# Kernel tuning notes

Hardware: AMD Instinct MI355X
Metric: run time of the kernel (lower is better)

## Reference

```python
import jax, jax.numpy as jnp
import numpy as np

NUM_GROUPS = 32
EPS = 1e-5


def group_norm(x, gamma, beta):
    b, c, h, w = x.shape
    xg = x.reshape(b, NUM_GROUPS, c // NUM_GROUPS, h, w)
    mu = xg.mean(axis=(2, 3, 4), keepdims=True)
    var = xg.var(axis=(2, 3, 4), keepdims=True)
    xg = (xg - mu) * jax.lax.rsqrt(var + EPS)
    x = xg.reshape(b, c, h, w)
    return x * gamma[None, :, None, None] + beta[None, :, None, None]


def conv1x1(x, w, b):
    # 1x1 conv == per-pixel matmul over channels
    return jnp.einsum('oc,bchw->bohw', w, x) + b[None, :, None, None]


def setup_inputs() -> dict:
    key = jax.random.key(0)
    ks = jax.random.split(key, 6)
    c = 512
    scale = 0.02  # keep logits in a sane range
    return {
        'x': jax.random.normal(ks[0], (2, c, 64, 64), dtype=jnp.float32),
        'gn_w': jnp.ones((c,), jnp.float32),
        'gn_b': jnp.zeros((c,), jnp.float32),
        'wq': jax.random.normal(ks[1], (c, c), jnp.float32) * scale,
        'bq': jnp.zeros((c,), jnp.float32),
        'wk': jax.random.normal(ks[2], (c, c), jnp.float32) * scale,
        'bk': jnp.zeros((c,), jnp.float32),
        'wv': jax.random.normal(ks[3], (c, c), jnp.float32) * scale,
        'bv': jnp.zeros((c,), jnp.float32),
        'wo': jax.random.normal(ks[4], (c, c), jnp.float32) * scale,
        'bo': jnp.zeros((c,), jnp.float32),
    }


def reference(x, gn_w, gn_b, wq, bq, wk, bk, wv, bv, wo, bo):
    b, c, h, w = x.shape
    n = h * w
    h_ = group_norm(x, gn_w, gn_b)
    q = conv1x1(h_, wq, bq).reshape(b, c, n)  # (b,c,n)
    k = conv1x1(h_, wk, bk).reshape(b, c, n)
    v = conv1x1(h_, wv, bv).reshape(b, c, n)
    # scores: (b, n_q, n_k) = q^T k, scaled by c^-0.5
    scores = jnp.einsum('bcq,bck->bqk', q, k) * (c ** -0.5)
    attn = jax.nn.softmax(scores, axis=-1)
    # h_ = v @ attn^T  -> (b, c, n_q)
    out = jnp.einsum('bck,bqk->bcq', v, attn).reshape(b, c, h, w)
    return x + conv1x1(out, wo, bo)
```

## Files before the change

### kernel.cpp

```cpp
#include <hip/hip_runtime.h>

typedef __bf16 bf16_t;
typedef __bf16 bf16x8 __attribute__((ext_vector_type(8)));
typedef __bf16 bf16x4 __attribute__((ext_vector_type(4)));
typedef float  floatx4 __attribute__((ext_vector_type(4)));

#define B_  2
#define C_  512
#define N_  4096
#define EPS 1e-5f
#define SCALE 0.044194173824159216f

__device__ __forceinline__ void gl2lds16(const void* g, void* l) {
  __builtin_amdgcn_global_load_lds(
      (const __attribute__((address_space(1))) void*)g,
      (__attribute__((address_space(3))) void*)l, 16, 0, 0);
}

__device__ __forceinline__ unsigned char f8(float x) {
  return (unsigned char)(__builtin_amdgcn_cvt_pk_fp8_f32(x, x, 0, false) & 0xff);
}

template <int BM, int BN>
__device__ __forceinline__ void gemm_main(
    const bf16_t* __restrict__ A, const bf16_t* __restrict__ B, int K,
    int m0, int n0, floatx4 (&acc)[BM / 32][BN / 32],
    bf16_t* __restrict__ As, bf16_t* __restrict__ Bs) {
  const int tid = threadIdx.x;
  const int w = tid >> 6, l = tid & 63;
  const int wm = (w >> 1) * (BM / 2), wn = (w & 1) * (BN / 2);
  const int lrow = l & 15, lq = l >> 4;
  const int key = lrow & 7;
  const int slot0 = lq ^ key;
  const int slot1 = (4 + lq) ^ key;

  floatx4 zero = {0.f, 0.f, 0.f, 0.f};
#pragma unroll
  for (int mm = 0; mm < BM / 32; mm++)
#pragma unroll
    for (int nn = 0; nn < BN / 32; nn++) acc[mm][nn] = zero;

  for (int k0 = 0; k0 < K; k0 += 64) {
#pragma unroll
    for (int p = 0; p < BM / 32; p++) {
      int gch = p * 256 + tid;
      int r = gch >> 3;
      int cg = (gch & 7) ^ (r & 7);
      gl2lds16(A + (size_t)(m0 + r) * K + k0 + cg * 8, As + gch * 8);
    }
#pragma unroll
    for (int p = 0; p < BN / 32; p++) {
      int gch = p * 256 + tid;
      int r = gch >> 3;
      int cg = (gch & 7) ^ (r & 7);
      gl2lds16(B + (size_t)(n0 + r) * K + k0 + cg * 8, Bs + gch * 8);
    }
    __syncthreads();

    bf16x8 af[BM / 32][2], bfr[BN / 32][2];
#pragma unroll
    for (int mm = 0; mm < BM / 32; mm++) {
      int row = wm + mm * 16 + lrow;
      af[mm][0] = *(const bf16x8*)(As + row * 64 + slot0 * 8);
      af[mm][1] = *(const bf16x8*)(As + row * 64 + slot1 * 8);
    }
#pragma unroll
    for (int nn = 0; nn < BN / 32; nn++) {
      int row = wn + nn * 16 + lrow;
      bfr[nn][0] = *(const bf16x8*)(Bs + row * 64 + slot0 * 8);
      bfr[nn][1] = *(const bf16x8*)(Bs + row * 64 + slot1 * 8);
    }
#pragma unroll
    for (int h = 0; h < 2; h++)
#pragma unroll
      for (int mm = 0; mm < BM / 32; mm++)
#pragma unroll
        for (int nn = 0; nn < BN / 32; nn++)
          acc[mm][nn] = __builtin_amdgcn_mfma_f32_16x16x32_bf16(
              af[mm][h], bfr[nn][h], acc[mm][nn], 0, 0, 0);
    __syncthreads();
  }
}

__global__ __launch_bounds__(256) void gemm_qkv(
    const bf16_t* __restrict__ Wqkv, const bf16_t* __restrict__ h_t,
    bf16_t* __restrict__ q_t, bf16_t* __restrict__ k_t,
    unsigned char* __restrict__ v8,
    const float* __restrict__ bq, const float* __restrict__ bk,
    const float* __restrict__ bv) {
  __shared__ __align__(16) char smem[32768];
  floatx4 acc[4][4];
  const int m0 = blockIdx.y * 128, n0 = blockIdx.x * 128;
  gemm_main<128, 128>(Wqkv, h_t, 512, m0, n0, acc,
                      (bf16_t*)smem, (bf16_t*)(smem + 16384));

  const int tid = threadIdx.x, w = tid >> 6, l = tid & 63;
  const int wm = (w >> 1) * 64, wn = (w & 1) * 64;
  const int lrow = l & 15, q4 = (l >> 4) * 4;
  const int mat = m0 >> 9;
  const float* bias = (mat == 0) ? bq : (mat == 1) ? bk : bv;

  if (mat < 2) {
    bf16_t* ot = (mat == 0) ? q_t : k_t;
#pragma unroll
    for (int mm = 0; mm < 4; mm++) {
#pragma unroll
      for (int nn = 0; nn < 4; nn++) {
        int n = n0 + wn + nn * 16 + lrow;
        int mloc = m0 - mat * 512 + wm + mm * 16 + q4;
        floatx4 a = acc[mm][nn];
        bf16x4 t;
#pragma unroll
        for (int r = 0; r < 4; r++) t[r] = (bf16_t)(a[r] + bias[mloc + r]);
        *(bf16x4*)(ot + (size_t)n * 512 + mloc) = t;
      }
    }
  } else {
    unsigned char* tile8 = (unsigned char*)smem;
#pragma unroll
    for (int mm = 0; mm < 4; mm++) {
#pragma unroll
      for (int nn = 0; nn < 4; nn++) {
        int colp = wn + nn * 16 + lrow;
        floatx4 a = acc[mm][nn];
#pragma unroll
        for (int r = 0; r < 4; r++) {
          int row = wm + mm * 16 + q4 + r;
          int ch = (colp >> 4) ^ ((row >> 2) & 7);
          tile8[row * 128 + ch * 16 + (colp & 15)] =
              f8(a[r] + bias[m0 - 1024 + row]);
        }
      }
    }
    __syncthreads();
    const int bb = n0 >> 12, nl0 = n0 & 4095;
    const int mloc0 = m0 - 1024;
#pragma unroll
    for (int i = 0; i < 4; i++) {
      int c = i * 256 + tid;
      int row = c >> 3, k = c & 7;
      int ch = k ^ ((row >> 2) & 7);
      uint4 d = *(const uint4*)(tile8 + row * 128 + ch * 16);
      *(uint4*)(v8 + (size_t)bb * (C_ * N_) + (size_t)(mloc0 + row) * N_ +
                nl0 + k * 16) = d;
    }
  }
}

__global__ __launch_bounds__(256) void gemm_scores(
    const bf16_t* __restrict__ q_t, const bf16_t* __restrict__ k_t,
    unsigned char* __restrict__ S8, size_t sstride, float* __restrict__ L,
    int zbase, int nz) {
  __shared__ __align__(16) char smem[32768];
  const int id = blockIdx.x;
  const int x = id & 7, s = id >> 3;
  const int mi = s & 3, n = (s >> 2) & 31;
  const int zloc = (nz == 2) ? (s >> 7) : 0;
  const int z = (nz == 2) ? zloc : zbase;
  const int m = x * 4 + mi;

  const bf16_t* A = k_t + (size_t)z * (N_ * C_);
  const bf16_t* B = q_t + (size_t)z * (N_ * C_);
  unsigned char* Sb = S8 + (size_t)zloc * sstride;
  float* Lb = L + (size_t)zloc * N_;
  floatx4 acc[4][4];
  const int m0 = m * 128, n0 = n * 128;
  gemm_main<128, 128>(A, B, 512, m0, n0, acc,
                      (bf16_t*)smem, (bf16_t*)(smem + 16384));

  const int tid = threadIdx.x, w = tid >> 6, l = tid & 63;
  const int wm = (w >> 1) * 64, wn = (w & 1) * 64;
  const int lrow = l & 15, lq = l >> 4;

  float lsum[4] = {0.f, 0.f, 0.f, 0.f};
#pragma unroll
  for (int mm = 0; mm < 4; mm++) {
#pragma unroll
    for (int nn = 0; nn < 4; nn++) {
      int i  = n0 + wn + nn * 16 + lrow;
      int jb = m0 + wm + mm * 16 + lq * 4;
      floatx4 a = acc[mm][nn];
      float e0 = __expf(a[0] * SCALE);
      float e1 = __expf(a[1] * SCALE);
      float e2 = __expf(a[2] * SCALE);
      float e3 = __expf(a[3] * SCALE);
      lsum[nn] += (e0 + e1) + (e2 + e3);
      unsigned int p = __builtin_amdgcn_cvt_pk_fp8_f32(e0, e1, 0, false);
      p = __builtin_amdgcn_cvt_pk_fp8_f32(e2, e3, p, true);
      *(unsigned int*)(Sb + (size_t)i * N_ + jb) = p;
    }
  }
#pragma unroll
  for (int nn = 0; nn < 4; nn++) {
    float vsum = lsum[nn];
    vsum += __shfl_xor(vsum, 16);
    vsum += __shfl_xor(vsum, 32);
    if (lq == 0)
      atomicAdd(Lb + n0 + wn + nn * 16 + lrow, vsum);
  }
}

__global__ __launch_bounds__(512) void gemm_pv(
    const unsigned char* __restrict__ S8, size_t sstride,
    const unsigned char* __restrict__ v8, const float* __restrict__ L,
    bf16_t* __restrict__ O_t, int zbase, int nz) {
  __shared__ __align__(16) char smem[49152];
  const int id = blockIdx.x;
  int nb, mb, zloc;
  if (nz == 2) { nb = id >> 6; int g = id & 63; mb = g >> 1; zloc = g & 1; }
  else         { nb = id >> 5; mb = id & 31; zloc = 0; }
  const int z = (nz == 2) ? zloc : zbase;

  const unsigned char* A = S8 + (size_t)zloc * sstride;
  const unsigned char* B = v8 + (size_t)z * (C_ * N_);
  const float* Lb = L + (size_t)zloc * N_;
  const int m0 = mb * 128, n0 = nb * 64;

  const int tid = threadIdx.x;
  const int w = tid >> 6, l = tid & 63;
  const int wk = w >> 2;
  const int wl = w & 3;
  const int t2 = tid & 255;
  unsigned char* Ah = (unsigned char*)smem + wk * (128 * 128);
  unsigned char* Bh = (unsigned char*)(smem + 32768) + wk * (64 * 128);

  const int wm = (wl >> 1) * 64, wn = (wl & 1) * 32;
  const int lrow = l & 15, lq = l >> 4;
  const int key = lrow & 7;
  const int fsub = (lq & 1) * 8;
  const int fc0 = ((0 + (lq >> 1)) ^ key) * 16 + fsub;
  const int fc1 = ((2 + (lq >> 1)) ^ key) * 16 + fsub;
  const int fc2 = ((4 + (lq >> 1)) ^ key) * 16 + fsub;
  const int fc3 = ((6 + (lq >> 1)) ^ key) * 16 + fsub;
  const int fo[4] = {fc0, fc1, fc2, fc3};

  floatx4 acc[4][2];
  floatx4 zero = {0.f, 0.f, 0.f, 0.f};
#pragma unroll
  for (int mm = 0; mm < 4; mm++)
#pragma unroll
    for (int nn = 0; nn < 2; nn++) acc[mm][nn] = zero;

  const int kbase = wk * 2048;
  for (int kk = 0; kk < 2048; kk += 128) {
    const int k0 = kbase + kk;
#pragma unroll
    for (int p = 0; p < 4; p++) {
      int gch = p * 256 + t2;
      int r = gch >> 3;
      int cg = (gch & 7) ^ (r & 7);
      gl2lds16(A + (size_t)(m0 + r) * 4096 + k0 + cg * 16, Ah + gch * 16);
    }
#pragma unroll
    for (int p = 0; p < 2; p++) {
      int gch = p * 256 + t2;
      int r = gch >> 3;
      int cg = (gch & 7) ^ (r & 7);
      gl2lds16(B + (size_t)(n0 + r) * 4096 + k0 + cg * 16, Bh + gch * 16);
    }
    __syncthreads();

    long af[4][4], bfr[2][4];
#pragma unroll
    for (int mm = 0; mm < 4; mm++) {
      int row = wm + mm * 16 + lrow;
#pragma unroll
      for (int h = 0; h < 4; h++)
        af[mm][h] = *(const long*)(Ah + row * 128 + fo[h]);
    }
#pragma unroll
    for (int nn = 0; nn < 2; nn++) {
      int row = wn + nn * 16 + lrow;
#pragma unroll
      for (int h = 0; h < 4; h++)
        bfr[nn][h] = *(const long*)(Bh + row * 128 + fo[h]);
    }
#pragma unroll
    for (int h = 0; h < 4; h++)
#pragma unroll
      for (int mm = 0; mm < 4; mm++)
#pragma unroll
        for (int nn = 0; nn < 2; nn++)
          acc[mm][nn] = __builtin_amdgcn_mfma_f32_16x16x32_fp8_fp8(
              af[mm][h], bfr[nn][h], acc[mm][nn], 0, 0, 0);
    __syncthreads();
  }

  floatx4* buf = (floatx4*)smem;
  const int lanebase = wl * 64 + l;
  if (wk == 1) {
#pragma unroll
    for (int mm = 0; mm < 4; mm++)
#pragma unroll
      for (int nn = 0; nn < 2; nn++)
        buf[(mm * 2 + nn) * 256 + lanebase] = acc[mm][nn];
  }
  __syncthreads();

  bf16_t* tile = (bf16_t*)(smem + 32768);
  if (wk == 0) {
    const int q4 = lq * 4;
#pragma unroll
    for (int mm = 0; mm < 4; mm++) {
      const int rowb = wm + mm * 16 + q4;
      float rv0 = 1.0f / Lb[m0 + rowb + 0];
      float rv1 = 1.0f / Lb[m0 + rowb + 1];
      float rv2 = 1.0f / Lb[m0 + rowb + 2];
      float rv3 = 1.0f / Lb[m0 + rowb + 3];
#pragma unroll
      for (int nn = 0; nn < 2; nn++) {
        floatx4 a = acc[mm][nn] + buf[(mm * 2 + nn) * 256 + lanebase];
        a[0] *= rv0; a[1] *= rv1; a[2] *= rv2; a[3] *= rv3;
        int colp = wn + nn * 16 + lrow;
#pragma unroll
        for (int r = 0; r < 4; r++) {
          int row = rowb + r;
          int ch = (colp >> 3) ^ ((row >> 2) & 7);
          tile[row * 64 + ch * 8 + (colp & 7)] = (bf16_t)a[r];
        }
      }
    }
  }
  __syncthreads();
#pragma unroll
  for (int i = 0; i < 2; i++) {
    int c = i * 512 + tid;
    int row = c >> 3, k = c & 7;
    int ch = k ^ ((row >> 2) & 7);
    bf16x8 d = *(const bf16x8*)(tile + row * 64 + ch * 8);
    *(bf16x8*)(O_t + ((size_t)z * N_ + m0 + row) * C_ + n0 + k * 8) = d;
  }
}

__global__ __launch_bounds__(256) void gemm_final(
    const bf16_t* __restrict__ wo, const bf16_t* __restrict__ O_t,
    const float* __restrict__ bo, const float* __restrict__ x,
    float* __restrict__ out) {
  __shared__ __align__(16) char smem[32768];
  floatx4 acc[2][4];
  const int m0 = blockIdx.y * 64, n0 = blockIdx.x * 128;
  gemm_main<64, 128>(wo, O_t, 512, m0, n0, acc,
                     (bf16_t*)smem, (bf16_t*)(smem + 8192));

  const int tid = threadIdx.x, w = tid >> 6, l = tid & 63;
  const int wm = (w >> 1) * 32, wn = (w & 1) * 64;
  const int lrow = l & 15, q4 = (l >> 4) * 4;

  float* tile = (float*)smem;
#pragma unroll
  for (int mm = 0; mm < 2; mm++) {
#pragma unroll
    for (int nn = 0; nn < 4; nn++) {
      int colp = wn + nn * 16 + lrow;
      floatx4 a = acc[mm][nn];
#pragma unroll
      for (int r = 0; r < 4; r++) {
        int row = wm + mm * 16 + q4 + r;
        int ch = (colp >> 2) ^ ((row >> 2) & 31);
        tile[row * 128 + ch * 4 + (colp & 3)] = a[r] + bo[m0 + row];
      }
    }
  }
  __syncthreads();
  const int bb = n0 >> 12, nl0 = n0 & 4095;
#pragma unroll
  for (int i = 0; i < 8; i++) {
    int c = i * 256 + tid;
    int row = c >> 5, k = c & 31;
    int ch = k ^ ((row >> 2) & 31);
    float4 dv = *(const float4*)(tile + row * 128 + ch * 4);
    size_t off = ((size_t)(bb * C_ + m0 + row)) * N_ + nl0 + k * 4;
    float4 xv = *(const float4*)(x + off);
    dv.x += xv.x; dv.y += xv.y; dv.z += xv.z; dv.w += xv.w;
    *(float4*)(out + off) = dv;
  }
}

__global__ __launch_bounds__(256) void prep_kernel(
    const float* __restrict__ s0, const float* __restrict__ s1,
    const float* __restrict__ s2, const float* __restrict__ s3,
    bf16_t* __restrict__ d_qkv, bf16_t* __restrict__ d_o,
    const float* __restrict__ x, float2* __restrict__ part,
    float* __restrict__ L) {
  const int id = blockIdx.x;
  const int tid = threadIdx.x;
  __shared__ float rs[4], rss[4];
  if (id < 4096) {
    int i = id * 256 + tid;
    int mat = i >> 18, idx = i & 262143;
    const float* s = (mat == 0) ? s0 : (mat == 1) ? s1 : (mat == 2) ? s2 : s3;
    if (mat < 3)
      d_qkv[mat * 262144 + idx] = (bf16_t)s[idx];
    else
      d_o[idx] = (bf16_t)s[idx];
  } else if (id < 4608) {
    const int sid = id - 4096;
    const float4* xp = (const float4*)(x + (size_t)sid * 8192);
    float s = 0.f, ss = 0.f;
#pragma unroll
    for (int i = 0; i < 8; i++) {
      float4 v = xp[tid + i * 256];
      s += v.x + v.y + v.z + v.w;
      ss += v.x * v.x + v.y * v.y + v.z * v.z + v.w * v.w;
    }
#pragma unroll
    for (int off = 32; off; off >>= 1) {
      s += __shfl_down(s, off);
      ss += __shfl_down(ss, off);
    }
    if ((tid & 63) == 0) { rs[tid >> 6] = s; rss[tid >> 6] = ss; }
    __syncthreads();
    if (tid == 0) {
      float2 p;
      p.x = rs[0] + rs[1] + rs[2] + rs[3];
      p.y = rss[0] + rss[1] + rss[2] + rss[3];
      part[sid] = p;
    }
  } else {
    float4 z4 = {0.f, 0.f, 0.f, 0.f};
    float4* Lp = (float4*)L;
#pragma unroll
    for (int i = 0; i < 8; i++) Lp[tid + i * 256] = z4;
  }
}

__global__ __launch_bounds__(256) void zeroL_kernel(float* __restrict__ L) {
  float4 z4 = {0.f, 0.f, 0.f, 0.f};
  ((float4*)L)[blockIdx.x * 256 + threadIdx.x] = z4;
}

__global__ __launch_bounds__(256) void gn_apply(
    const float* __restrict__ x, const float* __restrict__ gamma,
    const float* __restrict__ beta, const float2* __restrict__ part,
    bf16_t* __restrict__ h_t) {
  const int id = blockIdx.x;
  const int nc = id & 15, g = (id >> 4) & 31, b = id >> 9;
  const int bg = b * 32 + g;
  float s = 0.f, ss = 0.f;
#pragma unroll
  for (int i = 0; i < 8; i++) {
    float2 p = part[bg * 8 + i];
    s += p.x; ss += p.y;
  }
  const float mean = s * (1.f / 65536.f);
  const float inv = rsqrtf(ss * (1.f / 65536.f) - mean * mean + EPS);

  __shared__ bf16_t tile[256 * 17];
  const int tid = threadIdx.x;
  const int n0 = nc * 256;
#pragma unroll
  for (int i = 0; i < 4; i++) {
    int lin = i * 256 + tid;
    int cl = lin >> 6;
    int n4 = (lin & 63) * 4;
    int c = g * 16 + cl;
    float ga = gamma[c], be = beta[c];
    float4 v = *(const float4*)(x + ((size_t)(b * C_ + c)) * N_ + n0 + n4);
    tile[(n4 + 0) * 17 + cl] = (bf16_t)((v.x - mean) * inv * ga + be);
    tile[(n4 + 1) * 17 + cl] = (bf16_t)((v.y - mean) * inv * ga + be);
    tile[(n4 + 2) * 17 + cl] = (bf16_t)((v.z - mean) * inv * ga + be);
    tile[(n4 + 3) * 17 + cl] = (bf16_t)((v.w - mean) * inv * ga + be);
  }
  __syncthreads();
  union { bf16_t h[8]; uint4 u; } p0, p1;
#pragma unroll
  for (int c = 0; c < 8; c++)  p0.h[c] = tile[tid * 17 + c];
#pragma unroll
  for (int c = 0; c < 8; c++)  p1.h[c] = tile[tid * 17 + 8 + c];
  bf16_t* dst = h_t + ((size_t)(b * N_ + n0 + tid)) * C_ + g * 16;
  *(uint4*)dst = p0.u;
  *(uint4*)(dst + 8) = p1.u;
}

extern "C" void kernel_launch(void* const* d_in, const int* in_sizes, int n_in,
                              void* d_out, int out_size, void* d_ws, size_t ws_size,
                              hipStream_t stream) {
  const float* x    = (const float*)d_in[0];
  const float* gn_w = (const float*)d_in[1];
  const float* gn_b = (const float*)d_in[2];
  const float* wq   = (const float*)d_in[3];
  const float* bq   = (const float*)d_in[4];
  const float* wk   = (const float*)d_in[5];
  const float* bk   = (const float*)d_in[6];
  const float* wv   = (const float*)d_in[7];
  const float* bv   = (const float*)d_in[8];
  const float* wo   = (const float*)d_in[9];
  const float* bo   = (const float*)d_in[10];
  float* out = (float*)d_out;

  char* ws = (char*)d_ws;
  bf16_t* h_t  = (bf16_t*)(ws);
  bf16_t* q_t  = (bf16_t*)(ws + (8u << 20));
  bf16_t* k_t  = (bf16_t*)(ws + (16u << 20));
  unsigned char* v8 = (unsigned char*)(ws + (24u << 20));
  bf16_t* O_t  = (bf16_t*)(ws + (32u << 20));
  bf16_t* wqkv = (bf16_t*)(ws + (40u << 20));
  bf16_t* wob  = (bf16_t*)(ws + (42u << 20));
  float2* gnp  = (float2*)(ws + (43u << 20));
  float*  L    = (float*)(ws + (43u << 20) + 8192);
  unsigned char* S8 = (unsigned char*)(ws + (44u << 20));

  const size_t SN = (size_t)N_ * N_;
  const int nz = (ws_size >= (44u << 20) + 2 * SN) ? 2 : 1;

  prep_kernel<<<4609, 256, 0, stream>>>(wq, wk, wv, wo, wqkv, wob, x, gnp, L);
  gn_apply<<<1024, 256, 0, stream>>>(x, gn_w, gn_b, gnp, h_t);

  gemm_qkv<<<dim3(64, 12), 256, 0, stream>>>(wqkv, h_t, q_t, k_t, v8,
                                             bq, bk, bv);

  if (nz == 2) {
    gemm_scores<<<2048, 256, 0, stream>>>(q_t, k_t, S8, SN, L, 0, 2);
    gemm_pv<<<512, 512, 0, stream>>>(S8, SN, v8, L, O_t, 0, 2);
  } else {
    for (int b = 0; b < B_; b++) {
      zeroL_kernel<<<4, 256, 0, stream>>>(L);
      gemm_scores<<<1024, 256, 0, stream>>>(q_t, k_t, S8, 0, L, b, 1);
      gemm_pv<<<256, 512, 0, stream>>>(S8, 0, v8, L, O_t, b, 1);
    }
  }

  gemm_final<<<dim3(64, 8), 256, 0, stream>>>(wob, O_t, bo, x, out);
}
```

Measured before the change: 208.6 us.

## Store Q and K in FP8 and compute attention scores with FP8 MFMA

The QKV projection now writes Q and K as packed FP8 instead of bf16. The score GEMM is rewritten to load 128-wide FP8 K-tiles into swizzled LDS and accumulate with the fp8 16x16x32 MFMA. This halves Q/K memory traffic and uses the higher-throughput FP8 matrix path. In exchange it loses precision in the logits, which the exp/softmax then amplifies, so accuracy against the reference could suffer.

```diff
diff --git a/kernel.cpp b/kernel.cpp
--- a/kernel.cpp
+++ b/kernel.cpp
@@ -84,7 +84,7 @@
 
 __global__ __launch_bounds__(256) void gemm_qkv(
     const bf16_t* __restrict__ Wqkv, const bf16_t* __restrict__ h_t,
-    bf16_t* __restrict__ q_t, bf16_t* __restrict__ k_t,
+    unsigned char* __restrict__ q8, unsigned char* __restrict__ k8,
     unsigned char* __restrict__ v8,
     const float* __restrict__ bq, const float* __restrict__ bk,
     const float* __restrict__ bv) {
@@ -101,7 +101,7 @@
   const float* bias = (mat == 0) ? bq : (mat == 1) ? bk : bv;
 
   if (mat < 2) {
-    bf16_t* ot = (mat == 0) ? q_t : k_t;
+    unsigned char* ot = (mat == 0) ? q8 : k8;
 #pragma unroll
     for (int mm = 0; mm < 4; mm++) {
 #pragma unroll
@@ -109,10 +109,13 @@
         int n = n0 + wn + nn * 16 + lrow;
         int mloc = m0 - mat * 512 + wm + mm * 16 + q4;
         floatx4 a = acc[mm][nn];
-        bf16x4 t;
-#pragma unroll
-        for (int r = 0; r < 4; r++) t[r] = (bf16_t)(a[r] + bias[mloc + r]);
-        *(bf16x4*)(ot + (size_t)n * 512 + mloc) = t;
+        float v0 = a[0] + bias[mloc + 0];
+        float v1 = a[1] + bias[mloc + 1];
+        float v2 = a[2] + bias[mloc + 2];
+        float v3 = a[3] + bias[mloc + 3];
+        unsigned int p = __builtin_amdgcn_cvt_pk_fp8_f32(v0, v1, 0, false);
+        p = __builtin_amdgcn_cvt_pk_fp8_f32(v2, v3, p, true);
+        *(unsigned int*)(ot + (size_t)n * 512 + mloc) = p;
       }
     }
   } else {
@@ -148,29 +151,85 @@
 }
 
 __global__ __launch_bounds__(256) void gemm_scores(
-    const bf16_t* __restrict__ q_t, const bf16_t* __restrict__ k_t,
+    const unsigned char* __restrict__ q8, const unsigned char* __restrict__ k8,
     unsigned char* __restrict__ S8, size_t sstride, float* __restrict__ L,
     int zbase, int nz) {
-  __shared__ __align__(16) char smem[32768];
+  __shared__ __align__(16) unsigned char As[128 * 128];
+  __shared__ __align__(16) unsigned char Bs[128 * 128];
   const int id = blockIdx.x;
   const int x = id & 7, s = id >> 3;
   const int mi = s & 3, n = (s >> 2) & 31;
   const int zloc = (nz == 2) ? (s >> 7) : 0;
   const int z = (nz == 2) ? zloc : zbase;
   const int m = x * 4 + mi;
-
-  const bf16_t* A = k_t + (size_t)z * (N_ * C_);
-  const bf16_t* B = q_t + (size_t)z * (N_ * C_);
+  const int m0 = m * 128, n0 = n * 128;
+
+  const unsigned char* A = k8 + (size_t)z * (N_ * C_);
+  const unsigned char* B = q8 + (size_t)z * (N_ * C_);
   unsigned char* Sb = S8 + (size_t)zloc * sstride;
   float* Lb = L + (size_t)zloc * N_;
-  floatx4 acc[4][4];
-  const int m0 = m * 128, n0 = n * 128;
-  gemm_main<128, 128>(A, B, 512, m0, n0, acc,
-                      (bf16_t*)smem, (bf16_t*)(smem + 16384));
-
-  const int tid = threadIdx.x, w = tid >> 6, l = tid & 63;
+
+  const int tid = threadIdx.x;
+  const int w = tid >> 6, l = tid & 63;
   const int wm = (w >> 1) * 64, wn = (w & 1) * 64;
   const int lrow = l & 15, lq = l >> 4;
+  const int key = lrow & 7;
+  const int fsub = (lq & 1) * 8;
+  const int fo0 = ((0 + (lq >> 1)) ^ key) * 16 + fsub;
+  const int fo1 = ((2 + (lq >> 1)) ^ key) * 16 + fsub;
+  const int fo2 = ((4 + (lq >> 1)) ^ key) * 16 + fsub;
+  const int fo3 = ((6 + (lq >> 1)) ^ key) * 16 + fsub;
+  const int fo[4] = {fo0, fo1, fo2, fo3};
+
+  floatx4 acc[4][4];
+  floatx4 zero = {0.f, 0.f, 0.f, 0.f};
+#pragma unroll
+  for (int mm = 0; mm < 4; mm++)
+#pragma unroll
+    for (int nn = 0; nn < 4; nn++) acc[mm][nn] = zero;
+
+  for (int k0 = 0; k0 < C_; k0 += 128) {
+#pragma unroll
+    for (int p = 0; p < 4; p++) {
+      int gch = p * 256 + tid;
+      int r = gch >> 3;
+      int cg = (gch & 7) ^ (r & 7);
+      gl2lds16(A + (size_t)(m0 + r) * C_ + k0 + cg * 16, As + gch * 16);
+    }
+#pragma unroll
+    for (int p = 0; p < 4; p++) {
+      int gch = p * 256 + tid;
+      int r = gch >> 3;
+      int cg = (gch & 7) ^ (r & 7);
+      gl2lds16(B + (size_t)(n0 + r) * C_ + k0 + cg * 16, Bs + gch * 16);
+    }
+    __syncthreads();
+
+    long af[4][4], bfr[4][4];
+#pragma unroll
+    for (int mm = 0; mm < 4; mm++) {
+      int row = wm + mm * 16 + lrow;
+#pragma unroll
+      for (int h = 0; h < 4; h++)
+        af[mm][h] = *(const long*)(As + row * 128 + fo[h]);
+    }
+#pragma unroll
+    for (int nn = 0; nn < 4; nn++) {
+      int row = wn + nn * 16 + lrow;
+#pragma unroll
+      for (int h = 0; h < 4; h++)
+        bfr[nn][h] = *(const long*)(Bs + row * 128 + fo[h]);
+    }
+#pragma unroll
+    for (int h = 0; h < 4; h++)
+#pragma unroll
+      for (int mm = 0; mm < 4; mm++)
+#pragma unroll
+        for (int nn = 0; nn < 4; nn++)
+          acc[mm][nn] = __builtin_amdgcn_mfma_f32_16x16x32_fp8_fp8(
+              af[mm][h], bfr[nn][h], acc[mm][nn], 0, 0, 0);
+    __syncthreads();
+  }
 
   float lsum[4] = {0.f, 0.f, 0.f, 0.f};
 #pragma unroll
@@ -490,8 +549,8 @@
 
   char* ws = (char*)d_ws;
   bf16_t* h_t  = (bf16_t*)(ws);
-  bf16_t* q_t  = (bf16_t*)(ws + (8u << 20));
-  bf16_t* k_t  = (bf16_t*)(ws + (16u << 20));
+  unsigned char* q8 = (unsigned char*)(ws + (8u << 20));
+  unsigned char* k8 = (unsigned char*)(ws + (16u << 20));
   unsigned char* v8 = (unsigned char*)(ws + (24u << 20));
   bf16_t* O_t  = (bf16_t*)(ws + (32u << 20));
   bf16_t* wqkv = (bf16_t*)(ws + (40u << 20));
@@ -506,16 +565,16 @@
   prep_kernel<<<4609, 256, 0, stream>>>(wq, wk, wv, wo, wqkv, wob, x, gnp, L);
   gn_apply<<<1024, 256, 0, stream>>>(x, gn_w, gn_b, gnp, h_t);
 
-  gemm_qkv<<<dim3(64, 12), 256, 0, stream>>>(wqkv, h_t, q_t, k_t, v8,
+  gemm_qkv<<<dim3(64, 12), 256, 0, stream>>>(wqkv, h_t, q8, k8, v8,
                                              bq, bk, bv);
 
   if (nz == 2) {
-    gemm_scores<<<2048, 256, 0, stream>>>(q_t, k_t, S8, SN, L, 0, 2);
+    gemm_scores<<<2048, 256, 0, stream>>>(q8, k8, S8, SN, L, 0, 2);
     gemm_pv<<<512, 512, 0, stream>>>(S8, SN, v8, L, O_t, 0, 2);
   } else {
     for (int b = 0; b < B_; b++) {
       zeroL_kernel<<<4, 256, 0, stream>>>(L);
-      gemm_scores<<<1024, 256, 0, stream>>>(q_t, k_t, S8, 0, L, b, 1);
+      gemm_scores<<<1024, 256, 0, stream>>>(q8, k8, S8, 0, L, b, 1);
       gemm_pv<<<256, 512, 0, stream>>>(S8, 0, v8, L, O_t, b, 1);
     }
   }
```

Result: faster. 199.4 us (-4.4%).
